# Performance work log

Hardware: AMD Instinct MI355X
Metric: run time of the kernel (lower is better)

Reference implementation:

```python
import jax, jax.numpy as jnp
import numpy as np

N_NODES = 100000
N_EDGES = 1200000
VOCAB = 10000
EMBED = 32
HIDDEN = 64
N_CLASSES = 10
N_GRAPHS = 1024


def setup_inputs() -> dict:
    key = jax.random.key(0)
    ks = jax.random.split(key, 12)
    node_ids = jax.random.randint(ks[0], (N_NODES,), 0, VOCAB)
    src = jax.random.randint(ks[1], (N_EDGES,), 0, N_NODES)
    dst = jax.random.randint(ks[2], (N_EDGES,), 0, N_NODES)
    batch = jnp.sort(jax.random.randint(ks[3], (N_NODES,), 0, N_GRAPHS))
    s = lambda k, sh, fan: jax.random.normal(k, sh, jnp.float32) / np.sqrt(fan)
    return {
        "node_ids": node_ids, "src": src, "dst": dst, "batch": batch,
        "embed": s(ks[4], (VOCAB, EMBED), EMBED),
        "W1_l": s(ks[5], (EMBED, HIDDEN), EMBED), "b1": jnp.zeros((HIDDEN,), jnp.float32),
        "W1_r": s(ks[6], (EMBED, HIDDEN), EMBED),
        "W2_l": s(ks[7], (HIDDEN, HIDDEN), HIDDEN), "b2": jnp.zeros((HIDDEN,), jnp.float32),
        "W2_r": s(ks[8], (HIDDEN, HIDDEN), HIDDEN),
        "W_out": s(ks[9], (HIDDEN, N_CLASSES), HIDDEN), "b_out": jnp.zeros((N_CLASSES,), jnp.float32),
    }


def _sage(x, src, dst, W_l, b_l, W_r):
    # mean-aggregate neighbor (source) features at target nodes
    msg = jax.ops.segment_sum(x[src], dst, num_segments=N_NODES)  # [N, d]
    cnt = jax.ops.segment_sum(jnp.ones((src.shape[0],), x.dtype), dst, num_segments=N_NODES)
    agg = msg / jnp.maximum(cnt, 1.0)[:, None]
    # PyG SAGEConv: lin_l(aggr) (with bias) + lin_r(x) (no bias)
    return agg @ W_l + b_l + x @ W_r


def reference(node_ids, src, dst, batch, embed, W1_l, b1, W1_r, W2_l, b2, W2_r, W_out, b_out):
    x = embed[node_ids]                                   # [N, EMBED]
    x = jax.nn.relu(_sage(x, src, dst, W1_l, b1, W1_r))   # [N, HIDDEN]
    x = jax.nn.relu(_sage(x, src, dst, W2_l, b2, W2_r))   # [N, HIDDEN]
    # global mean pool over graphs
    gsum = jax.ops.segment_sum(x, batch, num_segments=N_GRAPHS)
    gcnt = jax.ops.segment_sum(jnp.ones((x.shape[0],), x.dtype), batch, num_segments=N_GRAPHS)
    pooled = gsum / jnp.maximum(gcnt, 1.0)[:, None]       # [G, HIDDEN]
    return pooled @ W_out + b_out                          # [G, N_CLASSES]
```

## Files before the change

### kernel.cpp

```cpp
#include <hip/hip_runtime.h>

#define EMBED 32
#define HIDDEN 64
#define NCLS 10


__global__ void deg_kernel(const int* __restrict__ dst, int* __restrict__ deg, int nEdges) {
    int e = blockIdx.x * blockDim.x + threadIdx.x;
    if (e >= nEdges) return;
    atomicAdd(&deg[dst[e]], 1);
}

__global__ void block_sum_kernel(const int* __restrict__ deg, int* __restrict__ blockSums, int n) {
    __shared__ int s[256];
    int i = blockIdx.x * 256 + threadIdx.x;
    s[threadIdx.x] = (i < n) ? deg[i] : 0;
    __syncthreads();
    for (int off = 128; off > 0; off >>= 1) {
        if (threadIdx.x < off) s[threadIdx.x] += s[threadIdx.x + off];
        __syncthreads();
    }
    if (threadIdx.x == 0) blockSums[blockIdx.x] = s[0];
}

__global__ void scan_sums_kernel(int* blockSums, int nb) {
    if (blockIdx.x == 0 && threadIdx.x == 0) {
        int acc = 0;
        for (int i = 0; i < nb; ++i) { int v = blockSums[i]; blockSums[i] = acc; acc += v; }
    }
}

__global__ void scan_local_kernel(const int* __restrict__ deg, const int* __restrict__ blockSums,
                                  int* __restrict__ rowptr, int n) {
    __shared__ int s[256];
    int i = blockIdx.x * 256 + threadIdx.x;
    int v = (i < n) ? deg[i] : 0;
    s[threadIdx.x] = v;
    __syncthreads();
    for (int off = 1; off < 256; off <<= 1) {
        int t = (threadIdx.x >= off) ? s[threadIdx.x - off] : 0;
        __syncthreads();
        s[threadIdx.x] += t;
        __syncthreads();
    }
    if (i < n) rowptr[i] = blockSums[blockIdx.x] + s[threadIdx.x] - v;
}

__global__ void fill_kernel(const int* __restrict__ src, const int* __restrict__ dst,
                            const int* __restrict__ rowptr, int* __restrict__ cursor,
                            int* __restrict__ nbr, int nEdges) {
    int e = blockIdx.x * blockDim.x + threadIdx.x;
    if (e >= nEdges) return;
    int d = dst[e];
    int pos = atomicAdd(&cursor[d], 1);
    nbr[rowptr[d] + pos] = src[e];
}

__launch_bounds__(512)
__global__ void layer1_fused(const int* __restrict__ nbr, const int* __restrict__ rowptr,
                             const int* __restrict__ deg, const int* __restrict__ node_ids,
                             const float* __restrict__ embed,
                             const float* __restrict__ W1l, const float* __restrict__ b1,
                             const float* __restrict__ W1r, float* __restrict__ h1, int nNodes) {
    __shared__ float sWl[EMBED * HIDDEN];
    __shared__ float sWr[EMBED * HIDDEN];

    int tid = threadIdx.x;
    for (int i = tid; i < EMBED * HIDDEN; i += 512) { sWl[i] = W1l[i]; sWr[i] = W1r[i]; }
    __syncthreads();

    int wave = tid >> 6;
    int lane = tid & 63;
    int half = lane >> 5;
    int f    = lane & 31;
    float bias = b1[lane];

    for (int n = blockIdx.x * 8 + wave; n < nNodes; n += gridDim.x * 8) {
        int dg = deg[n], start = rowptr[n];
        float xv = embed[(size_t)node_ids[n] * EMBED + f];

        float s0 = 0.f, s1 = 0.f;
        int j = half;
        for (; j + 2 < dg; j += 4) {
            int n0 = nbr[start + j];
            int n1 = nbr[start + j + 2];
            s0 += embed[(size_t)node_ids[n0] * EMBED + f];
            s1 += embed[(size_t)node_ids[n1] * EMBED + f];
        }
        for (; j < dg; j += 2)
            s0 += embed[(size_t)node_ids[nbr[start + j]] * EMBED + f];
        float sum = s0 + s1;
        sum += __shfl_xor(sum, 32);
        float aggv = sum / fmaxf((float)dg, 1.f);

        float acc = bias;
        #pragma unroll
        for (int k = 0; k < EMBED; ++k) {
            float a = __shfl(aggv, k);
            float x = __shfl(xv, k);
            acc += a * sWl[k * HIDDEN + lane] + x * sWr[k * HIDDEN + lane];
        }
        h1[(size_t)n * HIDDEN + lane] = fmaxf(acc, 0.f);
    }
}

__launch_bounds__(512)
__global__ void layer2_fused(const int* __restrict__ nbr, const int* __restrict__ rowptr,
                             const int* __restrict__ deg, const float* __restrict__ h1,
                             const float* __restrict__ W2l, const float* __restrict__ b2,
                             const float* __restrict__ W2r, const int* __restrict__ batch,
                             float* __restrict__ pooled, float* __restrict__ gcnt, int nNodes) {
    __shared__ float sWl[HIDDEN * HIDDEN];
    __shared__ float sWr[HIDDEN * HIDDEN];

    int tid = threadIdx.x;
    for (int i = tid; i < HIDDEN * HIDDEN; i += 512) { sWl[i] = W2l[i]; sWr[i] = W2r[i]; }
    __syncthreads();

    int wave = tid >> 6;
    int lane = tid & 63;
    float bias = b2[lane];

    for (int n = blockIdx.x * 8 + wave; n < nNodes; n += gridDim.x * 8) {
        int dg = deg[n], start = rowptr[n];
        int g = batch[n];
        float xv = h1[(size_t)n * HIDDEN + lane];

        float s0 = 0.f, s1 = 0.f, s2 = 0.f, s3 = 0.f;
        int j = 0;
        for (; j + 3 < dg; j += 4) {
            int n0 = nbr[start + j];
            int n1 = nbr[start + j + 1];
            int n2 = nbr[start + j + 2];
            int n3 = nbr[start + j + 3];
            s0 += h1[(size_t)n0 * HIDDEN + lane];
            s1 += h1[(size_t)n1 * HIDDEN + lane];
            s2 += h1[(size_t)n2 * HIDDEN + lane];
            s3 += h1[(size_t)n3 * HIDDEN + lane];
        }
        for (; j < dg; ++j)
            s0 += h1[(size_t)nbr[start + j] * HIDDEN + lane];
        float aggv = ((s0 + s1) + (s2 + s3)) / fmaxf((float)dg, 1.f);

        float acc = bias;
        #pragma unroll
        for (int k = 0; k < HIDDEN; ++k) {
            float a = __shfl(aggv, k);
            float x = __shfl(xv, k);
            acc += a * sWl[k * HIDDEN + lane] + x * sWr[k * HIDDEN + lane];
        }
        acc = fmaxf(acc, 0.f);
        atomicAdd(&pooled[(size_t)g * HIDDEN + lane], acc);
        if (lane == 0) atomicAdd(&gcnt[g], 1.f);
    }
}

__global__ void out_kernel(const float* __restrict__ pooled, const float* __restrict__ gcnt,
                           const float* __restrict__ Wout, const float* __restrict__ bout,
                           float* __restrict__ out, int nGraphs) {
    int i = blockIdx.x * blockDim.x + threadIdx.x;
    if (i >= nGraphs * NCLS) return;
    int g = i / NCLS;
    int c = i % NCLS;
    float inv = 1.0f / fmaxf(gcnt[g], 1.0f);
    float acc = bout[c];
    #pragma unroll
    for (int k = 0; k < HIDDEN; ++k)
        acc += pooled[(size_t)g * HIDDEN + k] * inv * Wout[k * NCLS + c];
    out[i] = acc;
}

extern "C" void kernel_launch(void* const* d_in, const int* in_sizes, int n_in,
                              void* d_out, int out_size, void* d_ws, size_t ws_size,
                              hipStream_t stream) {
    const int*   node_ids = (const int*)d_in[0];
    const int*   src      = (const int*)d_in[1];
    const int*   dst      = (const int*)d_in[2];
    const int*   batch    = (const int*)d_in[3];
    const float* embed    = (const float*)d_in[4];
    const float* W1l      = (const float*)d_in[5];
    const float* b1       = (const float*)d_in[6];
    const float* W1r      = (const float*)d_in[7];
    const float* W2l      = (const float*)d_in[8];
    const float* b2       = (const float*)d_in[9];
    const float* W2r      = (const float*)d_in[10];
    const float* Wout     = (const float*)d_in[11];
    const float* bout     = (const float*)d_in[12];

    const int N = in_sizes[0];
    const int E = in_sizes[1];
    const int G = out_size / NCLS;
    const int NB = (N + 255) / 256;

    int* deg       = (int*)d_ws;
    int* rowptr    = deg + N;
    int* cursor    = rowptr + N;
    int* blockSums = cursor + N;
    int* nbr       = blockSums + ((NB + 63) & ~63);
    float* h1      = (float*)(nbr + ((E + 63) & ~63));
    float* pooled  = h1 + (size_t)N * HIDDEN;
    float* gcnt    = pooled + (size_t)G * HIDDEN;

    float* out = (float*)d_out;

    hipMemsetAsync(deg, 0, (size_t)N * sizeof(int), stream);
    hipMemsetAsync(cursor, 0, (size_t)N * sizeof(int), stream);
    deg_kernel<<<(E + 255) / 256, 256, 0, stream>>>(dst, deg, E);
    block_sum_kernel<<<NB, 256, 0, stream>>>(deg, blockSums, N);
    scan_sums_kernel<<<1, 1, 0, stream>>>(blockSums, NB);
    scan_local_kernel<<<NB, 256, 0, stream>>>(deg, blockSums, rowptr, N);
    fill_kernel<<<(E + 255) / 256, 256, 0, stream>>>(src, dst, rowptr, cursor, nbr, E);

    layer1_fused<<<1024, 512, 0, stream>>>(nbr, rowptr, deg, node_ids, embed,
                                           W1l, b1, W1r, h1, N);

    hipMemsetAsync(pooled, 0, (size_t)G * HIDDEN * sizeof(float), stream);
    hipMemsetAsync(gcnt, 0, (size_t)G * sizeof(float), stream);
    layer2_fused<<<1024, 512, 0, stream>>>(nbr, rowptr, deg, h1, W2l, b2, W2r,
                                           batch, pooled, gcnt, N);

    out_kernel<<<(G * NCLS + 255) / 256, 256, 0, stream>>>(pooled, gcnt, Wout, bout, out, G);
}
```

Baseline: 641.5 us.

## Split SAGE layers into separate gather and update kernels

Each fused layer kernel is split into a latency-bound gather kernel, which writes mean-aggregated features to a workspace buffer using smaller 256-thread blocks, and a compute kernel that does the dense transform. The transform processes two nodes per wave and reads interleaved Wl/Wr weights as float2 from shared memory, halving LDS reads per FMA pair. The split is meant to let gathers run at higher occupancy, without the 16-32KB shared-memory weights limiting them. In exchange it adds an extra round trip of the aggregate buffer through global memory plus two extra launches, and it falls back to the fused path when the workspace is too small.

After: 768.3 us. 1.2x slower.

```diff
diff --git a/kernel.cpp b/kernel.cpp
--- a/kernel.cpp
+++ b/kernel.cpp
@@ -56,29 +56,17 @@
     nbr[rowptr[d] + pos] = src[e];
 }
 
-__launch_bounds__(512)
-__global__ void layer1_fused(const int* __restrict__ nbr, const int* __restrict__ rowptr,
-                             const int* __restrict__ deg, const int* __restrict__ node_ids,
-                             const float* __restrict__ embed,
-                             const float* __restrict__ W1l, const float* __restrict__ b1,
-                             const float* __restrict__ W1r, float* __restrict__ h1, int nNodes) {
-    __shared__ float sWl[EMBED * HIDDEN];
-    __shared__ float sWr[EMBED * HIDDEN];
-
-    int tid = threadIdx.x;
-    for (int i = tid; i < EMBED * HIDDEN; i += 512) { sWl[i] = W1l[i]; sWr[i] = W1r[i]; }
-    __syncthreads();
-
-    int wave = tid >> 6;
-    int lane = tid & 63;
-    int half = lane >> 5;
-    int f    = lane & 31;
-    float bias = b1[lane];
-
-    for (int n = blockIdx.x * 8 + wave; n < nNodes; n += gridDim.x * 8) {
+
+__launch_bounds__(256)
+__global__ void gather1_kernel(const int* __restrict__ nbr, const int* __restrict__ rowptr,
+                               const int* __restrict__ deg, const int* __restrict__ node_ids,
+                               const float* __restrict__ embed, float* __restrict__ agg1,
+                               int nNodes) {
+    int wave = threadIdx.x >> 6, lane = threadIdx.x & 63;
+    int half = lane >> 5, f = lane & 31;
+    int wid = blockIdx.x * 4 + wave, stride = gridDim.x * 4;
+    for (int n = wid; n < nNodes; n += stride) {
         int dg = deg[n], start = rowptr[n];
-        float xv = embed[(size_t)node_ids[n] * EMBED + f];
-
         float s0 = 0.f, s1 = 0.f;
         int j = half;
         for (; j + 2 < dg; j += 4) {
@@ -91,41 +79,56 @@
             s0 += embed[(size_t)node_ids[nbr[start + j]] * EMBED + f];
         float sum = s0 + s1;
         sum += __shfl_xor(sum, 32);
-        float aggv = sum / fmaxf((float)dg, 1.f);
-
-        float acc = bias;
+        if (half == 0) agg1[(size_t)n * EMBED + f] = sum / fmaxf((float)dg, 1.f);
+    }
+}
+
+__launch_bounds__(512)
+__global__ void update1_kernel(const float* __restrict__ agg1, const int* __restrict__ node_ids,
+                               const float* __restrict__ embed,
+                               const float* __restrict__ W1l, const float* __restrict__ b1,
+                               const float* __restrict__ W1r, float* __restrict__ h1, int nNodes) {
+    __shared__ float sW[EMBED * 2 * HIDDEN];
+    int tid = threadIdx.x;
+    for (int i = tid; i < EMBED * HIDDEN; i += 512) {
+        int k = i >> 6, c = i & 63;
+        sW[k * 128 + 2 * c]     = W1l[i];
+        sW[k * 128 + 2 * c + 1] = W1r[i];
+    }
+    __syncthreads();
+
+    int wave = tid >> 6, lane = tid & 63;
+    float bias = b1[lane];
+    int wid = blockIdx.x * 8 + wave, stride = gridDim.x * 8;
+    int nPairs = (nNodes + 1) >> 1;
+    for (int p = wid; p < nPairs; p += stride) {
+        int n0 = 2 * p, n1 = 2 * p + 1;
+        bool has1 = (n1 < nNodes);
+        float av0 = (lane < EMBED) ? agg1[(size_t)n0 * EMBED + lane]
+                                   : embed[(size_t)node_ids[n0] * EMBED + (lane - EMBED)];
+        float av1 = has1 ? ((lane < EMBED) ? agg1[(size_t)n1 * EMBED + lane]
+                                           : embed[(size_t)node_ids[n1] * EMBED + (lane - EMBED)])
+                         : 0.f;
+        float acc0 = bias, acc1 = bias;
         #pragma unroll
         for (int k = 0; k < EMBED; ++k) {
-            float a = __shfl(aggv, k);
-            float x = __shfl(xv, k);
-            acc += a * sWl[k * HIDDEN + lane] + x * sWr[k * HIDDEN + lane];
-        }
-        h1[(size_t)n * HIDDEN + lane] = fmaxf(acc, 0.f);
-    }
-}
-
-__launch_bounds__(512)
-__global__ void layer2_fused(const int* __restrict__ nbr, const int* __restrict__ rowptr,
-                             const int* __restrict__ deg, const float* __restrict__ h1,
-                             const float* __restrict__ W2l, const float* __restrict__ b2,
-                             const float* __restrict__ W2r, const int* __restrict__ batch,
-                             float* __restrict__ pooled, float* __restrict__ gcnt, int nNodes) {
-    __shared__ float sWl[HIDDEN * HIDDEN];
-    __shared__ float sWr[HIDDEN * HIDDEN];
-
-    int tid = threadIdx.x;
-    for (int i = tid; i < HIDDEN * HIDDEN; i += 512) { sWl[i] = W2l[i]; sWr[i] = W2r[i]; }
-    __syncthreads();
-
-    int wave = tid >> 6;
-    int lane = tid & 63;
-    float bias = b2[lane];
-
-    for (int n = blockIdx.x * 8 + wave; n < nNodes; n += gridDim.x * 8) {
+            float2 w = *(const float2*)&sW[k * 128 + 2 * lane];
+            acc0 += __shfl(av0, k) * w.x + __shfl(av0, EMBED + k) * w.y;
+            acc1 += __shfl(av1, k) * w.x + __shfl(av1, EMBED + k) * w.y;
+        }
+        h1[(size_t)n0 * HIDDEN + lane] = fmaxf(acc0, 0.f);
+        if (has1) h1[(size_t)n1 * HIDDEN + lane] = fmaxf(acc1, 0.f);
+    }
+}
+
+__launch_bounds__(256)
+__global__ void gather2_kernel(const int* __restrict__ nbr, const int* __restrict__ rowptr,
+                               const int* __restrict__ deg, const float* __restrict__ h1,
+                               float* __restrict__ agg2, int nNodes) {
+    int wave = threadIdx.x >> 6, lane = threadIdx.x & 63;
+    int wid = blockIdx.x * 4 + wave, stride = gridDim.x * 4;
+    for (int n = wid; n < nNodes; n += stride) {
         int dg = deg[n], start = rowptr[n];
-        int g = batch[n];
-        float xv = h1[(size_t)n * HIDDEN + lane];
-
         float s0 = 0.f, s1 = 0.f, s2 = 0.f, s3 = 0.f;
         int j = 0;
         for (; j + 3 < dg; j += 4) {
@@ -140,8 +143,130 @@
         }
         for (; j < dg; ++j)
             s0 += h1[(size_t)nbr[start + j] * HIDDEN + lane];
+        agg2[(size_t)n * HIDDEN + lane] = ((s0 + s1) + (s2 + s3)) / fmaxf((float)dg, 1.f);
+    }
+}
+
+__launch_bounds__(512)
+__global__ void update2_kernel(const float* __restrict__ agg2, const float* __restrict__ h1,
+                               const float* __restrict__ W2l, const float* __restrict__ b2,
+                               const float* __restrict__ W2r, const int* __restrict__ batch,
+                               float* __restrict__ pooled, float* __restrict__ gcnt, int nNodes) {
+    __shared__ float sW[HIDDEN * 2 * HIDDEN];
+    int tid = threadIdx.x;
+    for (int i = tid; i < HIDDEN * HIDDEN; i += 512) {
+        int k = i >> 6, c = i & 63;
+        sW[k * 128 + 2 * c]     = W2l[i];
+        sW[k * 128 + 2 * c + 1] = W2r[i];
+    }
+    __syncthreads();
+
+    int wave = tid >> 6, lane = tid & 63;
+    float bias = b2[lane];
+    int wid = blockIdx.x * 8 + wave, stride = gridDim.x * 8;
+    int nPairs = (nNodes + 1) >> 1;
+    for (int p = wid; p < nPairs; p += stride) {
+        int n0 = 2 * p, n1 = 2 * p + 1;
+        bool has1 = (n1 < nNodes);
+        float ag0 = agg2[(size_t)n0 * HIDDEN + lane];
+        float xv0 = h1[(size_t)n0 * HIDDEN + lane];
+        float ag1 = has1 ? agg2[(size_t)n1 * HIDDEN + lane] : 0.f;
+        float xv1 = has1 ? h1[(size_t)n1 * HIDDEN + lane] : 0.f;
+        float acc0 = bias, acc1 = bias;
+        #pragma unroll
+        for (int k = 0; k < HIDDEN; ++k) {
+            float2 w = *(const float2*)&sW[k * 128 + 2 * lane];
+            acc0 += __shfl(ag0, k) * w.x + __shfl(xv0, k) * w.y;
+            acc1 += __shfl(ag1, k) * w.x + __shfl(xv1, k) * w.y;
+        }
+        acc0 = fmaxf(acc0, 0.f);
+        int g0 = batch[n0];
+        atomicAdd(&pooled[(size_t)g0 * HIDDEN + lane], acc0);
+        if (has1) {
+            acc1 = fmaxf(acc1, 0.f);
+            int g1 = batch[n1];
+            atomicAdd(&pooled[(size_t)g1 * HIDDEN + lane], acc1);
+            if (lane == 0) { atomicAdd(&gcnt[g0], 1.f); atomicAdd(&gcnt[g1], 1.f); }
+        } else if (lane == 0) {
+            atomicAdd(&gcnt[g0], 1.f);
+        }
+    }
+}
+
+
+__launch_bounds__(512)
+__global__ void layer1_fused(const int* __restrict__ nbr, const int* __restrict__ rowptr,
+                             const int* __restrict__ deg, const int* __restrict__ node_ids,
+                             const float* __restrict__ embed,
+                             const float* __restrict__ W1l, const float* __restrict__ b1,
+                             const float* __restrict__ W1r, float* __restrict__ h1, int nNodes) {
+    __shared__ float sWl[EMBED * HIDDEN];
+    __shared__ float sWr[EMBED * HIDDEN];
+    int tid = threadIdx.x;
+    for (int i = tid; i < EMBED * HIDDEN; i += 512) { sWl[i] = W1l[i]; sWr[i] = W1r[i]; }
+    __syncthreads();
+    int wave = tid >> 6, lane = tid & 63;
+    int half = lane >> 5, f = lane & 31;
+    float bias = b1[lane];
+    for (int n = blockIdx.x * 8 + wave; n < nNodes; n += gridDim.x * 8) {
+        int dg = deg[n], start = rowptr[n];
+        float xv = embed[(size_t)node_ids[n] * EMBED + f];
+        float s0 = 0.f, s1 = 0.f;
+        int j = half;
+        for (; j + 2 < dg; j += 4) {
+            int n0 = nbr[start + j];
+            int n1 = nbr[start + j + 2];
+            s0 += embed[(size_t)node_ids[n0] * EMBED + f];
+            s1 += embed[(size_t)node_ids[n1] * EMBED + f];
+        }
+        for (; j < dg; j += 2)
+            s0 += embed[(size_t)node_ids[nbr[start + j]] * EMBED + f];
+        float sum = s0 + s1;
+        sum += __shfl_xor(sum, 32);
+        float aggv = sum / fmaxf((float)dg, 1.f);
+        float acc = bias;
+        #pragma unroll
+        for (int k = 0; k < EMBED; ++k) {
+            float a = __shfl(aggv, k);
+            float x = __shfl(xv, k);
+            acc += a * sWl[k * HIDDEN + lane] + x * sWr[k * HIDDEN + lane];
+        }
+        h1[(size_t)n * HIDDEN + lane] = fmaxf(acc, 0.f);
+    }
+}
+
+__launch_bounds__(512)
+__global__ void layer2_fused(const int* __restrict__ nbr, const int* __restrict__ rowptr,
+                             const int* __restrict__ deg, const float* __restrict__ h1,
+                             const float* __restrict__ W2l, const float* __restrict__ b2,
+                             const float* __restrict__ W2r, const int* __restrict__ batch,
+                             float* __restrict__ pooled, float* __restrict__ gcnt, int nNodes) {
+    __shared__ float sWl[HIDDEN * HIDDEN];
+    __shared__ float sWr[HIDDEN * HIDDEN];
+    int tid = threadIdx.x;
+    for (int i = tid; i < HIDDEN * HIDDEN; i += 512) { sWl[i] = W2l[i]; sWr[i] = W2r[i]; }
+    __syncthreads();
+    int wave = tid >> 6, lane = tid & 63;
+    float bias = b2[lane];
+    for (int n = blockIdx.x * 8 + wave; n < nNodes; n += gridDim.x * 8) {
+        int dg = deg[n], start = rowptr[n];
+        int g = batch[n];
+        float xv = h1[(size_t)n * HIDDEN + lane];
+        float s0 = 0.f, s1 = 0.f, s2 = 0.f, s3 = 0.f;
+        int j = 0;
+        for (; j + 3 < dg; j += 4) {
+            int n0 = nbr[start + j];
+            int n1 = nbr[start + j + 1];
+            int n2 = nbr[start + j + 2];
+            int n3 = nbr[start + j + 3];
+            s0 += h1[(size_t)n0 * HIDDEN + lane];
+            s1 += h1[(size_t)n1 * HIDDEN + lane];
+            s2 += h1[(size_t)n2 * HIDDEN + lane];
+            s3 += h1[(size_t)n3 * HIDDEN + lane];
+        }
+        for (; j < dg; ++j)
+            s0 += h1[(size_t)nbr[start + j] * HIDDEN + lane];
         float aggv = ((s0 + s1) + (s2 + s3)) / fmaxf((float)dg, 1.f);
-
         float acc = bias;
         #pragma unroll
         for (int k = 0; k < HIDDEN; ++k) {
@@ -200,6 +325,10 @@
     float* h1      = (float*)(nbr + ((E + 63) & ~63));
     float* pooled  = h1 + (size_t)N * HIDDEN;
     float* gcnt    = pooled + (size_t)G * HIDDEN;
+    float* agg     = gcnt + 64;
+
+    size_t need_split = ((char*)(agg + (size_t)N * HIDDEN)) - (char*)d_ws;
+    const bool use_split = (ws_size >= need_split);
 
     float* out = (float*)d_out;
 
@@ -211,13 +340,20 @@
     scan_local_kernel<<<NB, 256, 0, stream>>>(deg, blockSums, rowptr, N);
     fill_kernel<<<(E + 255) / 256, 256, 0, stream>>>(src, dst, rowptr, cursor, nbr, E);
 
-    layer1_fused<<<1024, 512, 0, stream>>>(nbr, rowptr, deg, node_ids, embed,
-                                           W1l, b1, W1r, h1, N);
-
     hipMemsetAsync(pooled, 0, (size_t)G * HIDDEN * sizeof(float), stream);
     hipMemsetAsync(gcnt, 0, (size_t)G * sizeof(float), stream);
-    layer2_fused<<<1024, 512, 0, stream>>>(nbr, rowptr, deg, h1, W2l, b2, W2r,
-                                           batch, pooled, gcnt, N);
+
+    if (use_split) {
+        gather1_kernel<<<2048, 256, 0, stream>>>(nbr, rowptr, deg, node_ids, embed, agg, N);
+        update1_kernel<<<1024, 512, 0, stream>>>(agg, node_ids, embed, W1l, b1, W1r, h1, N);
+        gather2_kernel<<<2048, 256, 0, stream>>>(nbr, rowptr, deg, h1, agg, N);
+        update2_kernel<<<1024, 512, 0, stream>>>(agg, h1, W2l, b2, W2r, batch, pooled, gcnt, N);
+    } else {
+        layer1_fused<<<1024, 512, 0, stream>>>(nbr, rowptr, deg, node_ids, embed,
+                                               W1l, b1, W1r, h1, N);
+        layer2_fused<<<1024, 512, 0, stream>>>(nbr, rowptr, deg, h1, W2l, b2, W2r,
+                                               batch, pooled, gcnt, N);
+    }
 
     out_kernel<<<(G * NCLS + 255) / 256, 256, 0, stream>>>(pooled, gcnt, Wout, bout, out, G);
 }
```

## Process two nodes per wave with interleaved weights and binary-search graph counts

Applied to the files above, without the earlier changes.

Each wave now handles two nodes. In layer 1 each 32-lane half gathers one node's neighbours, so a node's gather no longer needs a cross-half reduction. In layer 2 the gather loops of both nodes are interleaved for more memory-level parallelism. W_l and W_r are interleaved in shared memory so one float2 load feeds both nodes' matmuls, and pooled atomics are merged when both nodes share a graph. Graph counts come from a binary search over the sorted batch array instead of per-node atomics, which relies on batch being sorted (as the setup produces).

Measured after the change: 562.4 us. 12.3% less time.

```diff
diff --git a/kernel.cpp b/kernel.cpp
--- a/kernel.cpp
+++ b/kernel.cpp
@@ -56,51 +56,69 @@
     nbr[rowptr[d] + pos] = src[e];
 }
 
+__global__ void gcnt_kernel(const int* __restrict__ batch, float* __restrict__ gcnt,
+                            int nNodes, int nGraphs) {
+    int g = blockIdx.x * blockDim.x + threadIdx.x;
+    if (g >= nGraphs) return;
+    int lo = 0, hi = nNodes;
+    while (lo < hi) { int m = (lo + hi) >> 1; if (batch[m] < g) lo = m + 1; else hi = m; }
+    int lo2 = lo, hi2 = nNodes;
+    while (lo2 < hi2) { int m = (lo2 + hi2) >> 1; if (batch[m] <= g) lo2 = m + 1; else hi2 = m; }
+    gcnt[g] = (float)(lo2 - lo);
+}
+
 __launch_bounds__(512)
 __global__ void layer1_fused(const int* __restrict__ nbr, const int* __restrict__ rowptr,
                              const int* __restrict__ deg, const int* __restrict__ node_ids,
                              const float* __restrict__ embed,
                              const float* __restrict__ W1l, const float* __restrict__ b1,
                              const float* __restrict__ W1r, float* __restrict__ h1, int nNodes) {
-    __shared__ float sWl[EMBED * HIDDEN];
-    __shared__ float sWr[EMBED * HIDDEN];
-
+    __shared__ float sW[EMBED * 2 * HIDDEN];
     int tid = threadIdx.x;
-    for (int i = tid; i < EMBED * HIDDEN; i += 512) { sWl[i] = W1l[i]; sWr[i] = W1r[i]; }
-    __syncthreads();
-
-    int wave = tid >> 6;
-    int lane = tid & 63;
-    int half = lane >> 5;
-    int f    = lane & 31;
+    for (int i = tid; i < EMBED * HIDDEN; i += 512) {
+        int k = i >> 6, c = i & 63;
+        sW[k * 128 + 2 * c]     = W1l[i];
+        sW[k * 128 + 2 * c + 1] = W1r[i];
+    }
+    __syncthreads();
+
+    int wave = tid >> 6, lane = tid & 63;
+    int half = lane >> 5, f = lane & 31;
     float bias = b1[lane];
 
-    for (int n = blockIdx.x * 8 + wave; n < nNodes; n += gridDim.x * 8) {
-        int dg = deg[n], start = rowptr[n];
-        float xv = embed[(size_t)node_ids[n] * EMBED + f];
-
-        float s0 = 0.f, s1 = 0.f;
-        int j = half;
-        for (; j + 2 < dg; j += 4) {
-            int n0 = nbr[start + j];
-            int n1 = nbr[start + j + 2];
-            s0 += embed[(size_t)node_ids[n0] * EMBED + f];
-            s1 += embed[(size_t)node_ids[n1] * EMBED + f];
-        }
-        for (; j < dg; j += 2)
-            s0 += embed[(size_t)node_ids[nbr[start + j]] * EMBED + f];
-        float sum = s0 + s1;
-        sum += __shfl_xor(sum, 32);
-        float aggv = sum / fmaxf((float)dg, 1.f);
-
-        float acc = bias;
+    for (int p = blockIdx.x * 8 + wave; 2 * p < nNodes; p += gridDim.x * 8) {
+        int n0 = 2 * p, n1 = 2 * p + 1;
+        bool has1 = (n1 < nNodes);
+        int n = half ? n1 : n0;
+        bool valid = half ? has1 : true;
+        int dg = valid ? deg[n] : 0;
+        int st = valid ? rowptr[n] : 0;
+
+        float xv = valid ? embed[(size_t)node_ids[n] * EMBED + f] : 0.f;
+
+        float s0 = 0.f, s1 = 0.f, s2 = 0.f, s3 = 0.f;
+        int j = 0;
+        for (; j + 3 < dg; j += 4) {
+            int i0 = nbr[st + j], i1 = nbr[st + j + 1];
+            int i2 = nbr[st + j + 2], i3 = nbr[st + j + 3];
+            s0 += embed[(size_t)node_ids[i0] * EMBED + f];
+            s1 += embed[(size_t)node_ids[i1] * EMBED + f];
+            s2 += embed[(size_t)node_ids[i2] * EMBED + f];
+            s3 += embed[(size_t)node_ids[i3] * EMBED + f];
+        }
+        for (; j < dg; ++j)
+            s0 += embed[(size_t)node_ids[nbr[st + j]] * EMBED + f];
+        float aggv = ((s0 + s1) + (s2 + s3)) / fmaxf((float)dg, 1.f);
+
+        float acc0 = bias, acc1 = bias;
         #pragma unroll
         for (int k = 0; k < EMBED; ++k) {
-            float a = __shfl(aggv, k);
-            float x = __shfl(xv, k);
-            acc += a * sWl[k * HIDDEN + lane] + x * sWr[k * HIDDEN + lane];
-        }
-        h1[(size_t)n * HIDDEN + lane] = fmaxf(acc, 0.f);
+            float2 w = *(const float2*)&sW[k * 128 + 2 * lane];
+            acc0 += __shfl(aggv, k) * w.x + __shfl(xv, k) * w.y;
+            acc1 += __shfl(aggv, EMBED + k) * w.x + __shfl(xv, EMBED + k) * w.y;
+        }
+        h1[(size_t)n0 * HIDDEN + lane] = fmaxf(acc0, 0.f);
+        if (has1) h1[(size_t)n1 * HIDDEN + lane] = fmaxf(acc1, 0.f);
     }
 }
 
@@ -109,49 +127,86 @@
                              const int* __restrict__ deg, const float* __restrict__ h1,
                              const float* __restrict__ W2l, const float* __restrict__ b2,
                              const float* __restrict__ W2r, const int* __restrict__ batch,
-                             float* __restrict__ pooled, float* __restrict__ gcnt, int nNodes) {
-    __shared__ float sWl[HIDDEN * HIDDEN];
-    __shared__ float sWr[HIDDEN * HIDDEN];
-
+                             float* __restrict__ pooled, int nNodes) {
+    __shared__ float sW[HIDDEN * 2 * HIDDEN];
     int tid = threadIdx.x;
-    for (int i = tid; i < HIDDEN * HIDDEN; i += 512) { sWl[i] = W2l[i]; sWr[i] = W2r[i]; }
-    __syncthreads();
-
-    int wave = tid >> 6;
-    int lane = tid & 63;
+    for (int i = tid; i < HIDDEN * HIDDEN; i += 512) {
+        int k = i >> 6, c = i & 63;
+        sW[k * 128 + 2 * c]     = W2l[i];
+        sW[k * 128 + 2 * c + 1] = W2r[i];
+    }
+    __syncthreads();
+
+    int wave = tid >> 6, lane = tid & 63;
     float bias = b2[lane];
 
-    for (int n = blockIdx.x * 8 + wave; n < nNodes; n += gridDim.x * 8) {
-        int dg = deg[n], start = rowptr[n];
-        int g = batch[n];
-        float xv = h1[(size_t)n * HIDDEN + lane];
-
-        float s0 = 0.f, s1 = 0.f, s2 = 0.f, s3 = 0.f;
+    for (int p = blockIdx.x * 8 + wave; 2 * p < nNodes; p += gridDim.x * 8) {
+        int n0 = 2 * p, n1 = 2 * p + 1;
+        bool has1 = (n1 < nNodes);
+        int dg0 = deg[n0], st0 = rowptr[n0];
+        int dg1 = has1 ? deg[n1] : 0;
+        int st1 = has1 ? rowptr[n1] : 0;
+
+        float xv0 = h1[(size_t)n0 * HIDDEN + lane];
+        float xv1 = has1 ? h1[(size_t)n1 * HIDDEN + lane] : 0.f;
+
+        float s00 = 0.f, s01 = 0.f, s02 = 0.f, s03 = 0.f;
+        float s10 = 0.f, s11 = 0.f, s12 = 0.f, s13 = 0.f;
+        int m = dg0 < dg1 ? dg0 : dg1;
         int j = 0;
-        for (; j + 3 < dg; j += 4) {
-            int n0 = nbr[start + j];
-            int n1 = nbr[start + j + 1];
-            int n2 = nbr[start + j + 2];
-            int n3 = nbr[start + j + 3];
-            s0 += h1[(size_t)n0 * HIDDEN + lane];
-            s1 += h1[(size_t)n1 * HIDDEN + lane];
-            s2 += h1[(size_t)n2 * HIDDEN + lane];
-            s3 += h1[(size_t)n3 * HIDDEN + lane];
-        }
-        for (; j < dg; ++j)
-            s0 += h1[(size_t)nbr[start + j] * HIDDEN + lane];
-        float aggv = ((s0 + s1) + (s2 + s3)) / fmaxf((float)dg, 1.f);
-
-        float acc = bias;
-        #pragma unroll
+        for (; j + 3 < m; j += 4) {
+            int a0 = nbr[st0 + j], a1 = nbr[st0 + j + 1];
+            int a2 = nbr[st0 + j + 2], a3 = nbr[st0 + j + 3];
+            int c0 = nbr[st1 + j], c1 = nbr[st1 + j + 1];
+            int c2 = nbr[st1 + j + 2], c3 = nbr[st1 + j + 3];
+            s00 += h1[(size_t)a0 * HIDDEN + lane];
+            s01 += h1[(size_t)a1 * HIDDEN + lane];
+            s02 += h1[(size_t)a2 * HIDDEN + lane];
+            s03 += h1[(size_t)a3 * HIDDEN + lane];
+            s10 += h1[(size_t)c0 * HIDDEN + lane];
+            s11 += h1[(size_t)c1 * HIDDEN + lane];
+            s12 += h1[(size_t)c2 * HIDDEN + lane];
+            s13 += h1[(size_t)c3 * HIDDEN + lane];
+        }
+        int t = j;
+        for (; t + 1 < dg0; t += 2) {
+            int a0 = nbr[st0 + t], a1 = nbr[st0 + t + 1];
+            s00 += h1[(size_t)a0 * HIDDEN + lane];
+            s01 += h1[(size_t)a1 * HIDDEN + lane];
+        }
+        if (t < dg0) s00 += h1[(size_t)nbr[st0 + t] * HIDDEN + lane];
+        t = j;
+        for (; t + 1 < dg1; t += 2) {
+            int c0 = nbr[st1 + t], c1 = nbr[st1 + t + 1];
+            s10 += h1[(size_t)c0 * HIDDEN + lane];
+            s11 += h1[(size_t)c1 * HIDDEN + lane];
+        }
+        if (t < dg1) s10 += h1[(size_t)nbr[st1 + t] * HIDDEN + lane];
+
+        float ag0 = ((s00 + s01) + (s02 + s03)) / fmaxf((float)dg0, 1.f);
+        float ag1 = ((s10 + s11) + (s12 + s13)) / fmaxf((float)dg1, 1.f);
+
+        float acc0 = bias, acc1 = bias;
+        #pragma unroll 16
         for (int k = 0; k < HIDDEN; ++k) {
-            float a = __shfl(aggv, k);
-            float x = __shfl(xv, k);
-            acc += a * sWl[k * HIDDEN + lane] + x * sWr[k * HIDDEN + lane];
-        }
-        acc = fmaxf(acc, 0.f);
-        atomicAdd(&pooled[(size_t)g * HIDDEN + lane], acc);
-        if (lane == 0) atomicAdd(&gcnt[g], 1.f);
+            float2 w = *(const float2*)&sW[k * 128 + 2 * lane];
+            acc0 += __shfl(ag0, k) * w.x + __shfl(xv0, k) * w.y;
+            acc1 += __shfl(ag1, k) * w.x + __shfl(xv1, k) * w.y;
+        }
+        float a0 = fmaxf(acc0, 0.f);
+        int g0 = batch[n0];
+        if (has1) {
+            float a1 = fmaxf(acc1, 0.f);
+            int g1 = batch[n1];
+            if (g0 == g1) {
+                atomicAdd(&pooled[(size_t)g0 * HIDDEN + lane], a0 + a1);
+            } else {
+                atomicAdd(&pooled[(size_t)g0 * HIDDEN + lane], a0);
+                atomicAdd(&pooled[(size_t)g1 * HIDDEN + lane], a1);
+            }
+        } else {
+            atomicAdd(&pooled[(size_t)g0 * HIDDEN + lane], a0);
+        }
     }
 }
 
@@ -211,13 +266,14 @@
     scan_local_kernel<<<NB, 256, 0, stream>>>(deg, blockSums, rowptr, N);
     fill_kernel<<<(E + 255) / 256, 256, 0, stream>>>(src, dst, rowptr, cursor, nbr, E);
 
+    gcnt_kernel<<<(G + 255) / 256, 256, 0, stream>>>(batch, gcnt, N, G);
+    hipMemsetAsync(pooled, 0, (size_t)G * HIDDEN * sizeof(float), stream);
+
     layer1_fused<<<1024, 512, 0, stream>>>(nbr, rowptr, deg, node_ids, embed,
                                            W1l, b1, W1r, h1, N);
 
-    hipMemsetAsync(pooled, 0, (size_t)G * HIDDEN * sizeof(float), stream);
-    hipMemsetAsync(gcnt, 0, (size_t)G * sizeof(float), stream);
     layer2_fused<<<1024, 512, 0, stream>>>(nbr, rowptr, deg, h1, W2l, b2, W2r,
-                                           batch, pooled, gcnt, N);
+                                           batch, pooled, N);
 
     out_kernel<<<(G * NCLS + 255) / 256, 256, 0, stream>>>(pooled, gcnt, Wout, bout, out, G);
 }
```
